# Kernel tuning notes

Hardware: AMD Instinct MI355X
Metric: run time of the kernel (lower is better)

The kernel has to match this reference:

```python
import jax, jax.numpy as jnp
import numpy as np

EPS = 1e-9
# ((top,bottom),(left,right)) zero-pads for the 8 neighbor directions,
# matching torch nn.ZeroPad2d((l,r,t,b)) order gate1..gate8 in the source.
PADS = [((0, 2), (0, 2)), ((0, 2), (1, 1)), ((0, 2), (2, 0)),
        ((1, 1), (0, 2)), ((1, 1), (2, 0)),
        ((2, 0), (0, 2)), ((2, 0), (1, 1)), ((2, 0), (2, 0))]


def _pad8(x):
    # x: (B,H,W) -> (B,8,H+2,W+2): 8 directional zero-padded shifts
    return jnp.stack([jnp.pad(x, ((0, 0), tb, lr)) for tb, lr in PADS], axis=1)


def _affinity_normalization(guidance):
    # guidance: (B,8,H,W) -> gate_wb (B,8,H+2,W+2), gate_sum (B,H,W)
    gate_wb = jnp.stack(
        [jnp.pad(guidance[:, k], ((0, 0), tb, lr)) for k, (tb, lr) in enumerate(PADS)],
        axis=1)
    abs_weight = jnp.sum(jnp.abs(gate_wb), axis=1, keepdims=True)
    gate_wb = gate_wb / (abs_weight + EPS)
    gate_sum = jnp.sum(gate_wb, axis=1)[:, 1:-1, 1:-1]
    return gate_wb, gate_sum


def setup_inputs() -> dict:
    key = jax.random.key(0)
    k1, k2, k3, k4 = jax.random.split(key, 4)
    B, H, W = 2, 384, 1280
    guidance = jax.random.normal(k1, (B, 8, H, W), dtype=jnp.float32)
    blur_depth = jax.random.uniform(k2, (B, 1, H, W), dtype=jnp.float32) * 80.0
    valid = (jax.random.uniform(k3, (B, 1, H, W)) < 0.05).astype(jnp.float32)
    sparse_depth = valid * jax.random.uniform(k4, (B, 1, H, W), dtype=jnp.float32) * 80.0
    return {"guidance": guidance, "blur_depth": blur_depth,
            "sparse_depth": sparse_depth, "prop_time": 24}


def reference(guidance, blur_depth, sparse_depth, prop_time):
    # CSPN affinity-guided iterative propagation (norm_type='8sum')
    gate_wb, gate_sum = _affinity_normalization(guidance)
    raw = blur_depth[:, 0]                       # (B,H,W)
    sparse_mask = jnp.sign(sparse_depth[:, 0])   # (B,H,W), 1 where valid
    d = raw
    for _ in range(prop_time):
        # weighted sum over 8 padded neighbor shifts, then crop halo
        nws = jnp.sum(gate_wb * _pad8(d), axis=1)[:, 1:-1, 1:-1]
        d = (1.0 - gate_sum) * raw + nws
        d = (1.0 - sparse_mask) * d + sparse_mask * raw
    return d  # (B,H,W), matches result_depth.squeeze(1)
```

## Files before the change

### kernel.cpp

```cpp
#include <hip/hip_runtime.h>
#include <hip/hip_fp16.h>

static constexpr int Hh = 384;
static constexpr int Ww = 1280;
static constexpr int HW = Hh * Ww;
static constexpr int NPIX = 2 * HW;
static constexpr int TILE_I = 32;
static constexpr int TILE_J = 40;
static constexpr int S_STEPS = 8;
static constexpr int RI = TILE_I + 2 * S_STEPS;
static constexpr int RJ = TILE_J + 2 * S_STEPS;
static constexpr int RR = RI * RJ;
static constexpr int II = RI - 2;
static constexpr int IJ = RJ - 2;
static constexpr int NPAIR_ROW = IJ / 2;
static constexpr int NPAIR = II * NPAIR_ROW;
static constexpr int BLOCK = 512;
static constexpr int PPQ = (RR + BLOCK - 1) / BLOCK;
static constexpr int PPR = (NPAIR + BLOCK - 1) / BLOCK;
static constexpr int TI_T = Hh / TILE_I;
static constexpr int TJ_T = Ww / TILE_J;
static constexpr int GRID = 2 * TI_T * TJ_T;
static constexpr int NXCD = 8;
static constexpr int CHUNK = GRID / NXCD;
static constexpr float EPSF = 1e-9f;

__device__ __constant__ int DI_c[8] = { 1, 1, 1, 0, 0, -1, -1, -1 };
__device__ __constant__ int DJ_c[8] = { 1, 0, -1, 1, -1, 1, 0, -1 };

static __device__ __forceinline__ int iclamp(int v, int lo, int hi) {
    return min(max(v, lo), hi);
}

__global__ void affinity_norm(const float* __restrict__ g,
                              const float* __restrict__ raw,
                              const float* __restrict__ sparse,
                              __half* __restrict__ wbuf,
                              float* __restrict__ cbuf) {
    int idx = blockIdx.x * blockDim.x + threadIdx.x;
    if (idx >= NPIX) return;
    int b = idx / HW;
    int r = idx - b * HW;
    int i = r / Ww;
    int j = r - i * Ww;

    const float* gb = g + (size_t)b * 8 * HW;
    float v[8];
    float a = EPSF;
#pragma unroll
    for (int k = 0; k < 8; k++) {
        int ii = i + DI_c[k], jj = j + DJ_c[k];
        float gv = 0.0f;
        if (ii >= 0 && ii < Hh && jj >= 0 && jj < Ww)
            gv = gb[k * HW + ii * Ww + jj];
        v[k] = gv;
        a += fabsf(gv);
    }
    float inv = 1.0f / a, gs = 0.0f;
#pragma unroll
    for (int k = 0; k < 8; k++) { v[k] *= inv; gs += v[k]; }

    float rawv = raw[idx];
    bool m = sparse[idx] > 0.0f;
    cbuf[idx] = m ? rawv : (1.0f - gs) * rawv;
    __half wv[8];
#pragma unroll
    for (int k = 0; k < 8; k++) wv[k] = __float2half(m ? 0.0f : v[k]);
    *(float4*)(wbuf + (size_t)idx * 8) = *(const float4*)wv;
}

template <bool FIRST>
__global__ __launch_bounds__(BLOCK, 3)
void mega(
    const __half* __restrict__ wbuf,
    const float* __restrict__ cbuf,
    const float* blur,
    const float* din,
    float* __restrict__ dout)
{
    __shared__ float sd[2][RR];

    const int tid = threadIdx.x;
    int bx = ((int)blockIdx.x % NXCD) * CHUNK + (int)blockIdx.x / NXCD;
    const int tj = bx % TJ_T; bx /= TJ_T;
    const int ti = bx % TI_T;
    const int b  = bx / TI_T;
    const int oi = ti * TILE_I - S_STEPS;
    const int oj = tj * TILE_J - S_STEPS;

    const float* dinb = (FIRST ? blur : din) + (size_t)b * HW;

#pragma unroll
    for (int q = 0; q < PPQ; q++) {
        int p = tid + q * BLOCK;
        if (p < RR) {
            int ri = p / RJ, rj = p - ri * RJ;
            int gi = iclamp(oi + ri, 0, Hh - 1);
            int gj = iclamp(oj + rj, 0, Ww - 1);
            sd[0][p] = dinb[gi * Ww + gj];
        }
    }

    __half2 wp[PPR][8];
    float2  Cc[PPR];
    int     pr[PPR];
#pragma unroll
    for (int q = 0; q < PPR; q++) {
        int pi = tid + q * BLOCK;
        if (pi < NPAIR) {
            int r0 = pi / NPAIR_ROW;
            int c0 = pi - r0 * NPAIR_ROW;
            int ri = 1 + r0;
            int rj = 1 + 2 * c0;
            int p  = ri * RJ + rj;
            int rngr = min(ri, RI - 1 - ri);
            int rng0 = min(rngr, min(rj,     RJ - 1 - rj));
            int rng1 = min(rngr, min(rj + 1, RJ - 2 - rj));
            pr[q] = p | (max(rng0, rng1) << 16);
            int gi = iclamp(oi + ri, 0, Hh - 1);
            int gj0 = iclamp(oj + rj,     0, Ww - 1);
            int gj1 = iclamp(oj + rj + 1, 0, Ww - 1);
            int idx0 = b * HW + gi * Ww + gj0;
            int idx1 = b * HW + gi * Ww + gj1;
            float4 wA = *(const float4*)(wbuf + (size_t)idx0 * 8);
            float4 wB = *(const float4*)(wbuf + (size_t)idx1 * 8);
            const __half* ha = (const __half*)&wA;
            const __half* hb = (const __half*)&wB;
#pragma unroll
            for (int k = 0; k < 8; k++)
                wp[q][k] = __halves2half2(ha[k], hb[k]);
            Cc[q] = make_float2(cbuf[idx0], cbuf[idx1]);
        } else {
            pr[q] = 0;
            Cc[q] = make_float2(0.0f, 0.0f);
#pragma unroll
            for (int k = 0; k < 8; k++)
                wp[q][k] = __halves2half2(__float2half(0.0f), __float2half(0.0f));
        }
    }
    __syncthreads();

    int cur = 0;
#pragma unroll 1
    for (int s = 1; s < S_STEPS; ++s) {
        const float* s0 = sd[cur];
        float* s1 = sd[cur ^ 1];
#pragma unroll
        for (int q = 0; q < PPR; q++) {
            if ((pr[q] >> 16) >= s) {
                int p = pr[q] & 0xffff;
                float2 uA = *(const float2*)(s0 + p - RJ - 1);
                float2 uB = *(const float2*)(s0 + p - RJ + 1);
                float2 mA = *(const float2*)(s0 + p - 1);
                float2 mB = *(const float2*)(s0 + p + 1);
                float2 dA = *(const float2*)(s0 + p + RJ - 1);
                float2 dB = *(const float2*)(s0 + p + RJ + 1);
                float ax = Cc[q].x, ay = Cc[q].y;
                ax = fmaf(__low2float (wp[q][0]), dB.x, ax);
                ay = fmaf(__high2float(wp[q][0]), dB.y, ay);
                ax = fmaf(__low2float (wp[q][1]), dA.y, ax);
                ay = fmaf(__high2float(wp[q][1]), dB.x, ay);
                ax = fmaf(__low2float (wp[q][2]), dA.x, ax);
                ay = fmaf(__high2float(wp[q][2]), dA.y, ay);
                ax = fmaf(__low2float (wp[q][3]), mB.x, ax);
                ay = fmaf(__high2float(wp[q][3]), mB.y, ay);
                ax = fmaf(__low2float (wp[q][4]), mA.x, ax);
                ay = fmaf(__high2float(wp[q][4]), mA.y, ay);
                ax = fmaf(__low2float (wp[q][5]), uB.x, ax);
                ay = fmaf(__high2float(wp[q][5]), uB.y, ay);
                ax = fmaf(__low2float (wp[q][6]), uA.y, ax);
                ay = fmaf(__high2float(wp[q][6]), uB.x, ay);
                ax = fmaf(__low2float (wp[q][7]), uA.x, ax);
                ay = fmaf(__high2float(wp[q][7]), uA.y, ay);
                s1[p]     = ax;
                s1[p + 1] = ay;
            }
        }
        __syncthreads();
        cur ^= 1;
    }

    const float* s0 = sd[cur];
#pragma unroll
    for (int q = 0; q < PPR; q++) {
        if ((pr[q] >> 16) >= S_STEPS) {
            int p = pr[q] & 0xffff;
            float2 uA = *(const float2*)(s0 + p - RJ - 1);
            float2 uB = *(const float2*)(s0 + p - RJ + 1);
            float2 mA = *(const float2*)(s0 + p - 1);
            float2 mB = *(const float2*)(s0 + p + 1);
            float2 dA = *(const float2*)(s0 + p + RJ - 1);
            float2 dB = *(const float2*)(s0 + p + RJ + 1);
            float ax = Cc[q].x, ay = Cc[q].y;
            ax = fmaf(__low2float (wp[q][0]), dB.x, ax);
            ay = fmaf(__high2float(wp[q][0]), dB.y, ay);
            ax = fmaf(__low2float (wp[q][1]), dA.y, ax);
            ay = fmaf(__high2float(wp[q][1]), dB.x, ay);
            ax = fmaf(__low2float (wp[q][2]), dA.x, ax);
            ay = fmaf(__high2float(wp[q][2]), dA.y, ay);
            ax = fmaf(__low2float (wp[q][3]), mB.x, ax);
            ay = fmaf(__high2float(wp[q][3]), mB.y, ay);
            ax = fmaf(__low2float (wp[q][4]), mA.x, ax);
            ay = fmaf(__high2float(wp[q][4]), mA.y, ay);
            ax = fmaf(__low2float (wp[q][5]), uB.x, ax);
            ay = fmaf(__high2float(wp[q][5]), uB.y, ay);
            ax = fmaf(__low2float (wp[q][6]), uA.y, ax);
            ay = fmaf(__high2float(wp[q][6]), uB.x, ay);
            ax = fmaf(__low2float (wp[q][7]), uA.x, ax);
            ay = fmaf(__high2float(wp[q][7]), uA.y, ay);
            int ri = p / RJ, rj = p - ri * RJ;
            int gbase = b * HW + (oi + ri) * Ww + (oj + rj);
            if (rj >= S_STEPS && rj < RJ - S_STEPS)
                dout[gbase]     = ax;
            if (rj + 1 >= S_STEPS && rj + 1 < RJ - S_STEPS)
                dout[gbase + 1] = ay;
        }
    }
}

extern "C" void kernel_launch(void* const* d_in, const int* in_sizes, int n_in,
                              void* d_out, int out_size, void* d_ws, size_t ws_size,
                              hipStream_t stream) {
    const float* guidance = (const float*)d_in[0];
    const float* blur     = (const float*)d_in[1];
    const float* sparse   = (const float*)d_in[2];
    float* out = (float*)d_out;

    char* ws = (char*)d_ws;
    float* bufA = (float*)ws;
    float* bufB = bufA + NPIX;
    __half* wbuf = (__half*)(bufB + NPIX);
    float*  cbuf = (float*)(wbuf + (size_t)NPIX * 8);

    const int threads = 256;
    const int blocks = (NPIX + threads - 1) / threads;
    affinity_norm<<<blocks, threads, 0, stream>>>(guidance, blur, sparse, wbuf, cbuf);

    mega<true ><<<GRID, BLOCK, 0, stream>>>(wbuf, cbuf, blur, nullptr, bufA);
    mega<false><<<GRID, BLOCK, 0, stream>>>(wbuf, cbuf, nullptr, bufA, bufB);
    mega<false><<<GRID, BLOCK, 0, stream>>>(wbuf, cbuf, nullptr, bufB, out);
}
```

Before: 134.1 us.

## Halve block barriers by wave-local row ownership with redundant halo recompute

The tile grows to 48 rows, and each of the 8 waves owns 8 rows plus a 1-row overlap band. Two propagation steps now run per barrier: the first into a scratch buffer covering the wave's rows and halo, then a wave-local second step after only a block fence, followed by one __syncthreads. This cuts block-wide barriers per 8-step chunk from 7 to 3 and reduces halo overhead per tile. The cost is redundant compute on overlap rows, a third LDS buffer and lower occupancy (launch bounds 3→2). Correctness depends on a wave reading only the scratch rows it wrote itself.

```diff
diff --git a/kernel.cpp b/kernel.cpp
--- a/kernel.cpp
+++ b/kernel.cpp
@@ -5,19 +5,16 @@
 static constexpr int Ww = 1280;
 static constexpr int HW = Hh * Ww;
 static constexpr int NPIX = 2 * HW;
-static constexpr int TILE_I = 32;
+static constexpr int TILE_I = 48;
 static constexpr int TILE_J = 40;
 static constexpr int S_STEPS = 8;
 static constexpr int RI = TILE_I + 2 * S_STEPS;
 static constexpr int RJ = TILE_J + 2 * S_STEPS;
 static constexpr int RR = RI * RJ;
-static constexpr int II = RI - 2;
-static constexpr int IJ = RJ - 2;
-static constexpr int NPAIR_ROW = IJ / 2;
-static constexpr int NPAIR = II * NPAIR_ROW;
+static constexpr int NPAIR_ROW = (RJ - 2) / 2;
 static constexpr int BLOCK = 512;
-static constexpr int PPQ = (RR + BLOCK - 1) / BLOCK;
-static constexpr int PPR = (NPAIR + BLOCK - 1) / BLOCK;
+static constexpr int PPQ = RR / BLOCK;
+static constexpr int PPA = 5;
 static constexpr int TI_T = Hh / TILE_I;
 static constexpr int TJ_T = Ww / TILE_J;
 static constexpr int GRID = 2 * TI_T * TJ_T;
@@ -70,7 +67,7 @@
 }
 
 template <bool FIRST>
-__global__ __launch_bounds__(BLOCK, 3)
+__global__ __launch_bounds__(BLOCK, 2)
 void mega(
     const __half* __restrict__ wbuf,
     const float* __restrict__ cbuf,
@@ -78,9 +75,12 @@
     const float* din,
     float* __restrict__ dout)
 {
-    __shared__ float sd[2][RR];
-
-    const int tid = threadIdx.x;
+    __shared__ float b0[RR], b1[RR], b2[RR];
+
+    const int tid  = threadIdx.x;
+    const int wave = tid >> 6;
+    const int lane = tid & 63;
+
     int bx = ((int)blockIdx.x % NXCD) * CHUNK + (int)blockIdx.x / NXCD;
     const int tj = bx % TJ_T; bx /= TJ_T;
     const int ti = bx % TI_T;
@@ -93,31 +93,34 @@
 #pragma unroll
     for (int q = 0; q < PPQ; q++) {
         int p = tid + q * BLOCK;
-        if (p < RR) {
-            int ri = p / RJ, rj = p - ri * RJ;
-            int gi = iclamp(oi + ri, 0, Hh - 1);
-            int gj = iclamp(oj + rj, 0, Ww - 1);
-            sd[0][p] = dinb[gi * Ww + gj];
-        }
-    }
-
-    __half2 wp[PPR][8];
-    float2  Cc[PPR];
-    int     pr[PPR];
-#pragma unroll
-    for (int q = 0; q < PPR; q++) {
-        int pi = tid + q * BLOCK;
-        if (pi < NPAIR) {
-            int r0 = pi / NPAIR_ROW;
-            int c0 = pi - r0 * NPAIR_ROW;
-            int ri = 1 + r0;
+        int ri = p / RJ, rj = p - ri * RJ;
+        int gi = iclamp(oi + ri, 0, Hh - 1);
+        int gj = iclamp(oj + rj, 0, Ww - 1);
+        b0[p] = dinb[gi * Ww + gj];
+    }
+
+    const int rs = (wave == 0) ? 1 : 8 * wave - 1;
+    const int re = min(63, 8 * wave + 9);
+    const int npairs = (re - rs) * NPAIR_ROW;
+
+    __half2 wp[PPA][8];
+    float2  Cc[PPA];
+    int     pr[PPA];
+#pragma unroll
+    for (int q = 0; q < PPA; q++) {
+        int m = lane + 64 * q;
+        if (m < npairs) {
+            int r0 = m / NPAIR_ROW;
+            int c0 = m - r0 * NPAIR_ROW;
+            int ri = rs + r0;
             int rj = 1 + 2 * c0;
             int p  = ri * RJ + rj;
             int rngr = min(ri, RI - 1 - ri);
             int rng0 = min(rngr, min(rj,     RJ - 1 - rj));
             int rng1 = min(rngr, min(rj + 1, RJ - 2 - rj));
-            pr[q] = p | (max(rng0, rng1) << 16);
-            int gi = iclamp(oi + ri, 0, Hh - 1);
+            int inb  = ((ri >> 3) == wave) ? 1 : 0;
+            pr[q] = p | (max(rng0, rng1) << 16) | (inb << 27);
+            int gi  = iclamp(oi + ri, 0, Hh - 1);
             int gj0 = iclamp(oj + rj,     0, Ww - 1);
             int gj1 = iclamp(oj + rj + 1, 0, Ww - 1);
             int idx0 = b * HW + gi * Ww + gj0;
@@ -140,82 +143,74 @@
     }
     __syncthreads();
 
-    int cur = 0;
+#define PAIR_BODY(SRC, P, Q)                                           \
+    float2 uA = *(const float2*)((SRC) + (P) - RJ - 1);                \
+    float2 uB = *(const float2*)((SRC) + (P) - RJ + 1);                \
+    float2 mA = *(const float2*)((SRC) + (P) - 1);                     \
+    float2 mB = *(const float2*)((SRC) + (P) + 1);                     \
+    float2 dA = *(const float2*)((SRC) + (P) + RJ - 1);                \
+    float2 dB = *(const float2*)((SRC) + (P) + RJ + 1);                \
+    float ax = Cc[Q].x, ay = Cc[Q].y;                                  \
+    ax = fmaf(__low2float (wp[Q][0]), dB.x, ax);                       \
+    ay = fmaf(__high2float(wp[Q][0]), dB.y, ay);                       \
+    ax = fmaf(__low2float (wp[Q][1]), dA.y, ax);                       \
+    ay = fmaf(__high2float(wp[Q][1]), dB.x, ay);                       \
+    ax = fmaf(__low2float (wp[Q][2]), dA.x, ax);                       \
+    ay = fmaf(__high2float(wp[Q][2]), dA.y, ay);                       \
+    ax = fmaf(__low2float (wp[Q][3]), mB.x, ax);                       \
+    ay = fmaf(__high2float(wp[Q][3]), mB.y, ay);                       \
+    ax = fmaf(__low2float (wp[Q][4]), mA.x, ax);                       \
+    ay = fmaf(__high2float(wp[Q][4]), mA.y, ay);                       \
+    ax = fmaf(__low2float (wp[Q][5]), uB.x, ax);                       \
+    ay = fmaf(__high2float(wp[Q][5]), uB.y, ay);                       \
+    ax = fmaf(__low2float (wp[Q][6]), uA.y, ax);                       \
+    ay = fmaf(__high2float(wp[Q][6]), uB.x, ay);                       \
+    ax = fmaf(__low2float (wp[Q][7]), uA.x, ax);                       \
+    ay = fmaf(__high2float(wp[Q][7]), uA.y, ay);
+
 #pragma unroll 1
-    for (int s = 1; s < S_STEPS; ++s) {
-        const float* s0 = sd[cur];
-        float* s1 = sd[cur ^ 1];
-#pragma unroll
-        for (int q = 0; q < PPR; q++) {
-            if ((pr[q] >> 16) >= s) {
+    for (int g = 0; g < 4; ++g) {
+        const float* X = (g & 1) ? b2 : b0;
+        float* Z = (g & 1) ? b0 : b2;
+        const int sA = 2 * g + 1;
+
+#pragma unroll
+        for (int q = 0; q < PPA; q++) {
+            if (((pr[q] >> 16) & 0xff) >= sA) {
                 int p = pr[q] & 0xffff;
-                float2 uA = *(const float2*)(s0 + p - RJ - 1);
-                float2 uB = *(const float2*)(s0 + p - RJ + 1);
-                float2 mA = *(const float2*)(s0 + p - 1);
-                float2 mB = *(const float2*)(s0 + p + 1);
-                float2 dA = *(const float2*)(s0 + p + RJ - 1);
-                float2 dB = *(const float2*)(s0 + p + RJ + 1);
-                float ax = Cc[q].x, ay = Cc[q].y;
-                ax = fmaf(__low2float (wp[q][0]), dB.x, ax);
-                ay = fmaf(__high2float(wp[q][0]), dB.y, ay);
-                ax = fmaf(__low2float (wp[q][1]), dA.y, ax);
-                ay = fmaf(__high2float(wp[q][1]), dB.x, ay);
-                ax = fmaf(__low2float (wp[q][2]), dA.x, ax);
-                ay = fmaf(__high2float(wp[q][2]), dA.y, ay);
-                ax = fmaf(__low2float (wp[q][3]), mB.x, ax);
-                ay = fmaf(__high2float(wp[q][3]), mB.y, ay);
-                ax = fmaf(__low2float (wp[q][4]), mA.x, ax);
-                ay = fmaf(__high2float(wp[q][4]), mA.y, ay);
-                ax = fmaf(__low2float (wp[q][5]), uB.x, ax);
-                ay = fmaf(__high2float(wp[q][5]), uB.y, ay);
-                ax = fmaf(__low2float (wp[q][6]), uA.y, ax);
-                ay = fmaf(__high2float(wp[q][6]), uB.x, ay);
-                ax = fmaf(__low2float (wp[q][7]), uA.x, ax);
-                ay = fmaf(__high2float(wp[q][7]), uA.y, ay);
-                s1[p]     = ax;
-                s1[p + 1] = ay;
+                PAIR_BODY(X, p, q);
+                b1[p] = ax; b1[p + 1] = ay;
             }
         }
-        __syncthreads();
-        cur ^= 1;
-    }
-
-    const float* s0 = sd[cur];
-#pragma unroll
-    for (int q = 0; q < PPR; q++) {
-        if ((pr[q] >> 16) >= S_STEPS) {
-            int p = pr[q] & 0xffff;
-            float2 uA = *(const float2*)(s0 + p - RJ - 1);
-            float2 uB = *(const float2*)(s0 + p - RJ + 1);
-            float2 mA = *(const float2*)(s0 + p - 1);
-            float2 mB = *(const float2*)(s0 + p + 1);
-            float2 dA = *(const float2*)(s0 + p + RJ - 1);
-            float2 dB = *(const float2*)(s0 + p + RJ + 1);
-            float ax = Cc[q].x, ay = Cc[q].y;
-            ax = fmaf(__low2float (wp[q][0]), dB.x, ax);
-            ay = fmaf(__high2float(wp[q][0]), dB.y, ay);
-            ax = fmaf(__low2float (wp[q][1]), dA.y, ax);
-            ay = fmaf(__high2float(wp[q][1]), dB.x, ay);
-            ax = fmaf(__low2float (wp[q][2]), dA.x, ax);
-            ay = fmaf(__high2float(wp[q][2]), dA.y, ay);
-            ax = fmaf(__low2float (wp[q][3]), mB.x, ax);
-            ay = fmaf(__high2float(wp[q][3]), mB.y, ay);
-            ax = fmaf(__low2float (wp[q][4]), mA.x, ax);
-            ay = fmaf(__high2float(wp[q][4]), mA.y, ay);
-            ax = fmaf(__low2float (wp[q][5]), uB.x, ax);
-            ay = fmaf(__high2float(wp[q][5]), uB.y, ay);
-            ax = fmaf(__low2float (wp[q][6]), uA.y, ax);
-            ay = fmaf(__high2float(wp[q][6]), uB.x, ay);
-            ax = fmaf(__low2float (wp[q][7]), uA.x, ax);
-            ay = fmaf(__high2float(wp[q][7]), uA.y, ay);
-            int ri = p / RJ, rj = p - ri * RJ;
-            int gbase = b * HW + (oi + ri) * Ww + (oj + rj);
-            if (rj >= S_STEPS && rj < RJ - S_STEPS)
-                dout[gbase]     = ax;
-            if (rj + 1 >= S_STEPS && rj + 1 < RJ - S_STEPS)
-                dout[gbase + 1] = ay;
+        __threadfence_block();
+
+        if (g < 3) {
+#pragma unroll
+            for (int q = 0; q < PPA; q++) {
+                if ((pr[q] & (1 << 27)) && ((pr[q] >> 16) & 0xff) >= sA + 1) {
+                    int p = pr[q] & 0xffff;
+                    PAIR_BODY(b1, p, q);
+                    Z[p] = ax; Z[p + 1] = ay;
+                }
+            }
+            __syncthreads();
+        } else {
+#pragma unroll
+            for (int q = 0; q < PPA; q++) {
+                if ((pr[q] & (1 << 27)) && ((pr[q] >> 16) & 0xff) >= S_STEPS) {
+                    int p = pr[q] & 0xffff;
+                    PAIR_BODY(b1, p, q);
+                    int ri = p / RJ, rj = p - ri * RJ;
+                    int gbase = b * HW + (oi + ri) * Ww + (oj + rj);
+                    if (rj >= S_STEPS && rj < RJ - S_STEPS)
+                        dout[gbase]     = ax;
+                    if (rj + 1 >= S_STEPS && rj + 1 < RJ - S_STEPS)
+                        dout[gbase + 1] = ay;
+                }
+            }
         }
     }
+#undef PAIR_BODY
 }
 
 extern "C" void kernel_launch(void* const* d_in, const int* in_sizes, int n_in,
```

New measurement: 154.5 us. +15.2%, slower.
